# Kernel optimization log

Hardware: AMD Instinct MI355X
Metric: run time of the kernel (lower is better)

## Reference

```python
import jax, jax.numpy as jnp
import numpy as np

WINDOW_SIZE = 35

def setup_inputs() -> dict:
    key = jax.random.key(0)
    k1, k2 = jax.random.split(key)
    B, T, U = 4096, WINDOW_SIZE, 1024
    x = jax.random.normal(k1, (B, T, U), dtype=jnp.float32)
    # nn.Linear(units*2, units): weight [units, units*2], bias [units]
    W = jax.random.normal(k2, (U, 2 * U), dtype=jnp.float32) * (1.0 / np.sqrt(2 * U))
    b = jnp.zeros((U,), dtype=jnp.float32)
    return {"x": x, "W": W, "b": b}

def reference(x, W, b):
    # x: [B, T, U]; hidden init zeros [B, U]
    B, T, U = x.shape
    # split weight into input part and hidden part (concat order: [x_t, h])
    Wx = W[:, :U]   # [U, U]
    Wh = W[:, U:]   # [U, U]

    def step(h, x_t):
        # out = relu([x_t, h] @ W^T + b)
        h_new = jax.nn.relu(x_t @ Wx.T + h @ Wh.T + b)
        return h_new, None

    h0 = jnp.zeros((B, U), dtype=x.dtype)
    x_time_major = jnp.swapaxes(x, 0, 1)  # [T, B, U]
    h_final, _ = jax.lax.scan(step, h0, x_time_major)
    return h_final
```

## Files before the change

kernel.cpp:

```cpp
#include <hip/hip_runtime.h>


typedef __bf16 bf16;
typedef __bf16 bf16x8 __attribute__((ext_vector_type(8)));
typedef __bf16 bf16x4 __attribute__((ext_vector_type(4)));
typedef float f32x4 __attribute__((ext_vector_type(4)));

#define B_N 4096
#define T_N 35
#define U_N 1024
#define XROW (T_N * U_N)
#define BU (B_N * U_N)

#define AS1CP(p) ((const __attribute__((address_space(1))) void*)(p))
#define AS3CP(p) ((__attribute__((address_space(3))) void*)(p))

__global__ __launch_bounds__(256) void pack_w(const float* __restrict__ W,
                                              bf16* __restrict__ Wxb,
                                              bf16* __restrict__ Whb) {
  int i = (blockIdx.x * 256 + threadIdx.x) * 4;
  int n = i >> 10, k = i & 1023;
  f32x4 a = *(const f32x4*)(W + (size_t)n * 2048 + k);
  f32x4 b = *(const f32x4*)(W + (size_t)n * 2048 + 1024 + k);
  bf16x4 av = { (bf16)a.x, (bf16)a.y, (bf16)a.z, (bf16)a.w };
  bf16x4 bv = { (bf16)b.x, (bf16)b.y, (bf16)b.z, (bf16)b.w };
  *(bf16x4*)(Wxb + i) = av;
  *(bf16x4*)(Whb + i) = bv;
}

__global__ __launch_bounds__(256) void z_gemm(
    const float* __restrict__ x, const bf16* __restrict__ Wxb,
    const float* __restrict__ bias, bf16* __restrict__ Zb)
{
  __shared__ bf16 As[128 * 64];
  __shared__ bf16 Bs[128 * 64];

  const int tid = threadIdx.x;
  const int w = tid >> 6, l = tid & 63;
  const int mt = blockIdx.y;
  const int t = mt >> 5;
  const int row0 = (mt & 31) << 7;
  const int col0 = blockIdx.x << 7;
  const int wm = w & 1, wn = w >> 1;
  const int lq = l >> 4, lm = l & 15;
  const int lrow8 = l >> 3, lc = l & 7;
  const int clog = lc ^ lrow8;

  f32x4 acc[4][4] = {};
  const float* xbase = x + (size_t)row0 * XROW + (size_t)t * U_N;

  for (int kk = 0; kk < 1024; kk += 64) {
#pragma unroll
    for (int r = 0; r < 4; ++r) {
      int nr = w * 32 + r * 8;
      const bf16* g = Wxb + (size_t)(col0 + nr + lrow8) * U_N + kk + clog * 8;
      __builtin_amdgcn_global_load_lds(AS1CP(g), AS3CP(Bs + nr * 64), 16, 0, 0);
    }
#pragma unroll
    for (int i = 0; i < 4; ++i) {
      int row = i * 32 + (tid >> 3);
      int c = tid & 7;
      const float* g = xbase + (size_t)row * XROW + kk + c * 8;
      f32x4 f0 = *(const f32x4*)g;
      f32x4 f1 = *(const f32x4*)(g + 4);
      bf16x8 v = { (bf16)f0.x, (bf16)f0.y, (bf16)f0.z, (bf16)f0.w,
                   (bf16)f1.x, (bf16)f1.y, (bf16)f1.z, (bf16)f1.w };
      *(bf16x8*)(As + row * 64 + ((c ^ (row & 7)) << 3)) = v;
    }
    __syncthreads();

#pragma unroll
    for (int kq = 0; kq < 2; ++kq) {
      bf16x8 af[4], bfr[4];
#pragma unroll
      for (int mi = 0; mi < 4; ++mi) {
        int r = wm * 64 + mi * 16 + lm;
        af[mi] = *(const bf16x8*)(As + r * 64 + (((kq * 4 + lq) ^ (r & 7)) << 3));
      }
#pragma unroll
      for (int ni = 0; ni < 4; ++ni) {
        int r = wn * 64 + ni * 16 + lm;
        bfr[ni] = *(const bf16x8*)(Bs + r * 64 + (((kq * 4 + lq) ^ (r & 7)) << 3));
      }
#pragma unroll
      for (int mi = 0; mi < 4; ++mi)
#pragma unroll
        for (int ni = 0; ni < 4; ++ni)
          acc[mi][ni] = __builtin_amdgcn_mfma_f32_16x16x32_bf16(af[mi], bfr[ni],
                                                                acc[mi][ni], 0, 0, 0);
    }
    __syncthreads();
  }

#pragma unroll
  for (int ni = 0; ni < 4; ++ni) {
    int col = col0 + wn * 64 + ni * 16 + lm;
    float bv = bias[col];
#pragma unroll
    for (int mi = 0; mi < 4; ++mi) {
      int rbase = row0 + wm * 64 + mi * 16 + lq * 4;
#pragma unroll
      for (int i = 0; i < 4; ++i)
        Zb[(size_t)t * BU + (size_t)(rbase + i) * U_N + col] = (bf16)(acc[mi][ni][i] + bv);
    }
  }
}

__global__ __launch_bounds__(256) void rnn_step(
    const bf16* __restrict__ hin, const bf16* __restrict__ Whb,
    const bf16* __restrict__ Zt, bf16* __restrict__ hout,
    float* __restrict__ out)
{
  __shared__ bf16 As[128 * 64];
  __shared__ bf16 Bs[64 * 64];

  const int tid = threadIdx.x;
  const int w = tid >> 6, l = tid & 63;
  const int col0 = blockIdx.x << 6;
  const int row0 = blockIdx.y << 7;
  const int wm = w & 1, wn = w >> 1;
  const int lq = l >> 4, lm = l & 15;
  const int lrow8 = l >> 3, lc = l & 7;
  const int clog = lc ^ lrow8;

  f32x4 acc[4][2] = {};

  for (int kk = 0; kk < 1024; kk += 64) {
#pragma unroll
    for (int r = 0; r < 4; ++r) {
      int nr = w * 32 + r * 8;
      const bf16* g = hin + (size_t)(row0 + nr + lrow8) * U_N + kk + clog * 8;
      __builtin_amdgcn_global_load_lds(AS1CP(g), AS3CP(As + nr * 64), 16, 0, 0);
    }
#pragma unroll
    for (int r = 0; r < 2; ++r) {
      int nr = w * 16 + r * 8;
      const bf16* g = Whb + (size_t)(col0 + nr + lrow8) * U_N + kk + clog * 8;
      __builtin_amdgcn_global_load_lds(AS1CP(g), AS3CP(Bs + nr * 64), 16, 0, 0);
    }
    __syncthreads();

#pragma unroll
    for (int kq = 0; kq < 2; ++kq) {
      bf16x8 af[4], bfr[2];
#pragma unroll
      for (int mi = 0; mi < 4; ++mi) {
        int r = wm * 64 + mi * 16 + lm;
        af[mi] = *(const bf16x8*)(As + r * 64 + (((kq * 4 + lq) ^ (r & 7)) << 3));
      }
#pragma unroll
      for (int ni = 0; ni < 2; ++ni) {
        int r = wn * 32 + ni * 16 + lm;
        bfr[ni] = *(const bf16x8*)(Bs + r * 64 + (((kq * 4 + lq) ^ (r & 7)) << 3));
      }
#pragma unroll
      for (int mi = 0; mi < 4; ++mi)
#pragma unroll
        for (int ni = 0; ni < 2; ++ni)
          acc[mi][ni] = __builtin_amdgcn_mfma_f32_16x16x32_bf16(af[mi], bfr[ni],
                                                                acc[mi][ni], 0, 0, 0);
    }
    __syncthreads();
  }

#pragma unroll
  for (int ni = 0; ni < 2; ++ni) {
    int col = col0 + wn * 32 + ni * 16 + lm;
#pragma unroll
    for (int mi = 0; mi < 4; ++mi) {
      int rbase = row0 + wm * 64 + mi * 16 + lq * 4;
#pragma unroll
      for (int i = 0; i < 4; ++i) {
        int row = rbase + i;
        float v = acc[mi][ni][i] + (float)Zt[(size_t)row * U_N + col];
        v = v > 0.f ? v : 0.f;
        hout[(size_t)row * U_N + col] = (bf16)v;
        if (out) out[(size_t)row * U_N + col] = v;
      }
    }
  }
}

extern "C" void kernel_launch(void* const* d_in, const int* in_sizes, int n_in,
                              void* d_out, int out_size, void* d_ws, size_t ws_size,
                              hipStream_t stream) {
  const float* x    = (const float*)d_in[0];
  const float* W    = (const float*)d_in[1];
  const float* bias = (const float*)d_in[2];
  float* out = (float*)d_out;

  char* ws = (char*)d_ws;
  bf16* Wxb = (bf16*)ws;
  bf16* Whb = (bf16*)(ws + ((size_t)2 << 20));
  bf16* h0  = (bf16*)(ws + ((size_t)4 << 20));
  bf16* h1  = (bf16*)(ws + ((size_t)12 << 20));
  bf16* Zb  = (bf16*)(ws + ((size_t)32 << 20));

  pack_w<<<1024, 256, 0, stream>>>(W, Wxb, Whb);
  hipMemsetAsync(h0, 0, (size_t)BU * sizeof(bf16), stream);

  z_gemm<<<dim3(8, 1120), 256, 0, stream>>>(x, Wxb, bias, Zb);

  bf16* bufs[2] = { h0, h1 };
  for (int t = 0; t < T_N; ++t) {
    bf16* hin  = bufs[t & 1];
    bf16* hout = bufs[(t + 1) & 1];
    float* o   = (t == T_N - 1) ? out : nullptr;
    rnn_step<<<dim3(16, 32), 256, 0, stream>>>(hin, Whb, Zb + (size_t)t * BU, hout, o);
  }
}
```

Baseline: 2.237 ms.

## Fuse input projection and recurrence into one persistent cooperative kernel

Replaces the separate Z precompute GEMM and per-timestep launches with one cooperative persistent kernel. Each step computes [x_t, h] @ W^T over K=2048 with double-buffered LDS and split-K across two wave groups, and a global atomic barrier separates timesteps. This removes the Z intermediate's write and read traffic plus per-step launch overhead. In exchange the x projection is now on the serial per-step path, and the spin barrier adds synchronization cost.

```diff
diff --git a/kernel.cpp b/kernel.cpp
--- a/kernel.cpp
+++ b/kernel.cpp
@@ -9,174 +9,189 @@
 #define B_N 4096
 #define T_N 35
 #define U_N 1024
+#define K2 2048
 #define XROW (T_N * U_N)
-#define BU (B_N * U_N)
 
 #define AS1CP(p) ((const __attribute__((address_space(1))) void*)(p))
 #define AS3CP(p) ((__attribute__((address_space(3))) void*)(p))
 
 __global__ __launch_bounds__(256) void pack_w(const float* __restrict__ W,
-                                              bf16* __restrict__ Wxb,
-                                              bf16* __restrict__ Whb) {
+                                              bf16* __restrict__ Wb) {
   int i = (blockIdx.x * 256 + threadIdx.x) * 4;
-  int n = i >> 10, k = i & 1023;
-  f32x4 a = *(const f32x4*)(W + (size_t)n * 2048 + k);
-  f32x4 b = *(const f32x4*)(W + (size_t)n * 2048 + 1024 + k);
-  bf16x4 av = { (bf16)a.x, (bf16)a.y, (bf16)a.z, (bf16)a.w };
-  bf16x4 bv = { (bf16)b.x, (bf16)b.y, (bf16)b.z, (bf16)b.w };
-  *(bf16x4*)(Wxb + i) = av;
-  *(bf16x4*)(Whb + i) = bv;
+  f32x4 a = *(const f32x4*)(W + i);
+  bf16x4 v = { (bf16)a.x, (bf16)a.y, (bf16)a.z, (bf16)a.w };
+  *(bf16x4*)(Wb + i) = v;
 }
 
-__global__ __launch_bounds__(256) void z_gemm(
-    const float* __restrict__ x, const bf16* __restrict__ Wxb,
-    const float* __restrict__ bias, bf16* __restrict__ Zb)
+__global__ __launch_bounds__(512, 1) void rnn_fused(
+    const float* __restrict__ x, const bf16* __restrict__ Wb,
+    const float* __restrict__ bias, bf16* __restrict__ hA,
+    bf16* __restrict__ hB, float* __restrict__ out,
+    unsigned* __restrict__ bar, int t0, int t1)
 {
-  __shared__ bf16 As[128 * 64];
-  __shared__ bf16 Bs[128 * 64];
+  __shared__ __align__(16) bf16 smem[2][2][128 * 64];
 
   const int tid = threadIdx.x;
   const int w = tid >> 6, l = tid & 63;
-  const int mt = blockIdx.y;
-  const int t = mt >> 5;
-  const int row0 = (mt & 31) << 7;
-  const int col0 = blockIdx.x << 7;
-  const int wm = w & 1, wn = w >> 1;
+  const int L = blockIdx.x;
+  const int rg = (L & 7) * 4 + ((L >> 3) >> 3);
+  const int cg = (L >> 3) & 7;
+  const int r0 = rg << 7;
+  const int c0 = cg << 7;
+
+  const int s = w & 3;
+  const int g = w >> 2;
+  const int wm = s & 1, wn = s >> 1;
   const int lq = l >> 4, lm = l & 15;
-  const int lrow8 = l >> 3, lc = l & 7;
-  const int clog = lc ^ lrow8;
-
-  f32x4 acc[4][4] = {};
-  const float* xbase = x + (size_t)row0 * XROW + (size_t)t * U_N;
-
-  for (int kk = 0; kk < 1024; kk += 64) {
-#pragma unroll
-    for (int r = 0; r < 4; ++r) {
-      int nr = w * 32 + r * 8;
-      const bf16* g = Wxb + (size_t)(col0 + nr + lrow8) * U_N + kk + clog * 8;
-      __builtin_amdgcn_global_load_lds(AS1CP(g), AS3CP(Bs + nr * 64), 16, 0, 0);
-    }
-#pragma unroll
-    for (int i = 0; i < 4; ++i) {
-      int row = i * 32 + (tid >> 3);
-      int c = tid & 7;
-      const float* g = xbase + (size_t)row * XROW + kk + c * 8;
-      f32x4 f0 = *(const f32x4*)g;
-      f32x4 f1 = *(const f32x4*)(g + 4);
-      bf16x8 v = { (bf16)f0.x, (bf16)f0.y, (bf16)f0.z, (bf16)f0.w,
-                   (bf16)f1.x, (bf16)f1.y, (bf16)f1.z, (bf16)f1.w };
-      *(bf16x8*)(As + row * 64 + ((c ^ (row & 7)) << 3)) = v;
-    }
-    __syncthreads();
-
-#pragma unroll
-    for (int kq = 0; kq < 2; ++kq) {
-      bf16x8 af[4], bfr[4];
-#pragma unroll
-      for (int mi = 0; mi < 4; ++mi) {
-        int r = wm * 64 + mi * 16 + lm;
-        af[mi] = *(const bf16x8*)(As + r * 64 + (((kq * 4 + lq) ^ (r & 7)) << 3));
-      }
-#pragma unroll
-      for (int ni = 0; ni < 4; ++ni) {
-        int r = wn * 64 + ni * 16 + lm;
-        bfr[ni] = *(const bf16x8*)(Bs + r * 64 + (((kq * 4 + lq) ^ (r & 7)) << 3));
-      }
-#pragma unroll
-      for (int mi = 0; mi < 4; ++mi)
-#pragma unroll
-        for (int ni = 0; ni < 4; ++ni)
-          acc[mi][ni] = __builtin_amdgcn_mfma_f32_16x16x32_bf16(af[mi], bfr[ni],
-                                                                acc[mi][ni], 0, 0, 0);
-    }
-    __syncthreads();
-  }
-
-#pragma unroll
-  for (int ni = 0; ni < 4; ++ni) {
-    int col = col0 + wn * 64 + ni * 16 + lm;
-    float bv = bias[col];
-#pragma unroll
-    for (int mi = 0; mi < 4; ++mi) {
-      int rbase = row0 + wm * 64 + mi * 16 + lq * 4;
-#pragma unroll
-      for (int i = 0; i < 4; ++i)
-        Zb[(size_t)t * BU + (size_t)(rbase + i) * U_N + col] = (bf16)(acc[mi][ni][i] + bv);
-    }
-  }
-}
-
-__global__ __launch_bounds__(256) void rnn_step(
-    const bf16* __restrict__ hin, const bf16* __restrict__ Whb,
-    const bf16* __restrict__ Zt, bf16* __restrict__ hout,
-    float* __restrict__ out)
-{
-  __shared__ bf16 As[128 * 64];
-  __shared__ bf16 Bs[64 * 64];
-
-  const int tid = threadIdx.x;
-  const int w = tid >> 6, l = tid & 63;
-  const int col0 = blockIdx.x << 6;
-  const int row0 = blockIdx.y << 7;
-  const int wm = w & 1, wn = w >> 1;
-  const int lq = l >> 4, lm = l & 15;
-  const int lrow8 = l >> 3, lc = l & 7;
-  const int clog = lc ^ lrow8;
-
-  f32x4 acc[4][2] = {};
-
-  for (int kk = 0; kk < 1024; kk += 64) {
-#pragma unroll
-    for (int r = 0; r < 4; ++r) {
-      int nr = w * 32 + r * 8;
-      const bf16* g = hin + (size_t)(row0 + nr + lrow8) * U_N + kk + clog * 8;
-      __builtin_amdgcn_global_load_lds(AS1CP(g), AS3CP(As + nr * 64), 16, 0, 0);
-    }
+  const int lrow8 = l >> 3;
+  const int clog = (l & 7) ^ lrow8;
+
+  const int xrow = tid >> 2;
+  const int xc2 = tid & 3;
+  const float* xrowp = x + (size_t)(r0 + xrow) * XROW + xc2 * 16;
+
+  float bv[4];
+#pragma unroll
+  for (int ni = 0; ni < 4; ++ni) bv[ni] = bias[c0 + wn * 64 + ni * 16 + lm];
+
+  for (int t = t0; t < t1; ++t) {
+    const bf16* hin = (t & 1) ? hB : hA;
+    bf16* hout = (t & 1) ? hA : hB;
+    const int kend = (t == 0) ? 1024 : K2;
+    const float* xb = xrowp + (size_t)t * U_N;
+
+    f32x4 acc[4][4] = {};
+
 #pragma unroll
     for (int r = 0; r < 2; ++r) {
       int nr = w * 16 + r * 8;
-      const bf16* g = Whb + (size_t)(col0 + nr + lrow8) * U_N + kk + clog * 8;
-      __builtin_amdgcn_global_load_lds(AS1CP(g), AS3CP(Bs + nr * 64), 16, 0, 0);
+      const bf16* gb = Wb + (size_t)(c0 + nr + lrow8) * K2 + clog * 8;
+      __builtin_amdgcn_global_load_lds(AS1CP(gb), AS3CP(&smem[0][1][nr * 64]), 16, 0, 0);
+    }
+    {
+      f32x4 f0 = *(const f32x4*)(xb);
+      f32x4 f1 = *(const f32x4*)(xb + 4);
+      f32x4 f2 = *(const f32x4*)(xb + 8);
+      f32x4 f3 = *(const f32x4*)(xb + 12);
+      bf16x8 v0 = { (bf16)f0.x, (bf16)f0.y, (bf16)f0.z, (bf16)f0.w,
+                    (bf16)f1.x, (bf16)f1.y, (bf16)f1.z, (bf16)f1.w };
+      bf16x8 v1 = { (bf16)f2.x, (bf16)f2.y, (bf16)f2.z, (bf16)f2.w,
+                    (bf16)f3.x, (bf16)f3.y, (bf16)f3.z, (bf16)f3.w };
+      *(bf16x8*)(&smem[0][0][xrow * 64 + (((xc2 << 1) ^ (xrow & 7)) << 3)]) = v0;
+      *(bf16x8*)(&smem[0][0][xrow * 64 + ((((xc2 << 1) | 1) ^ (xrow & 7)) << 3)]) = v1;
     }
     __syncthreads();
 
-#pragma unroll
-    for (int kq = 0; kq < 2; ++kq) {
-      bf16x8 af[4], bfr[2];
-#pragma unroll
-      for (int mi = 0; mi < 4; ++mi) {
-        int r = wm * 64 + mi * 16 + lm;
-        af[mi] = *(const bf16x8*)(As + r * 64 + (((kq * 4 + lq) ^ (r & 7)) << 3));
-      }
-#pragma unroll
-      for (int ni = 0; ni < 2; ++ni) {
-        int r = wn * 32 + ni * 16 + lm;
-        bfr[ni] = *(const bf16x8*)(Bs + r * 64 + (((kq * 4 + lq) ^ (r & 7)) << 3));
-      }
+    int cur = 0;
+    for (int kk = 0; kk < kend; kk += 64) {
+      const int nkk = kk + 64;
+      const bool hasnext = nkk < kend;
+      const bool nx = hasnext && (nkk < 1024);
+      const bool nh = hasnext && (nkk >= 1024);
+      const int nxt = cur ^ 1;
+
+      f32x4 f0, f1, f2, f3;
+      if (nx) {
+        const float* gx = xb + nkk;
+        f0 = *(const f32x4*)(gx);
+        f1 = *(const f32x4*)(gx + 4);
+        f2 = *(const f32x4*)(gx + 8);
+        f3 = *(const f32x4*)(gx + 12);
+      }
+      if (hasnext) {
+#pragma unroll
+        for (int r = 0; r < 2; ++r) {
+          int nr = w * 16 + r * 8;
+          const bf16* gb = Wb + (size_t)(c0 + nr + lrow8) * K2 + nkk + clog * 8;
+          __builtin_amdgcn_global_load_lds(AS1CP(gb), AS3CP(&smem[nxt][1][nr * 64]), 16, 0, 0);
+        }
+      }
+      if (nh) {
+#pragma unroll
+        for (int r = 0; r < 2; ++r) {
+          int nr = w * 16 + r * 8;
+          const bf16* gh = hin + (size_t)(r0 + nr + lrow8) * U_N + (nkk - 1024) + clog * 8;
+          __builtin_amdgcn_global_load_lds(AS1CP(gh), AS3CP(&smem[nxt][0][nr * 64]), 16, 0, 0);
+        }
+      }
+
+      {
+        const bf16* As = &smem[cur][0][0];
+        const bf16* Bs = &smem[cur][1][0];
+        bf16x8 af[4], bfr[4];
+#pragma unroll
+        for (int mi = 0; mi < 4; ++mi) {
+          int r = wm * 64 + mi * 16 + lm;
+          af[mi] = *(const bf16x8*)(As + r * 64 + ((((g << 2) + lq) ^ (r & 7)) << 3));
+        }
+#pragma unroll
+        for (int ni = 0; ni < 4; ++ni) {
+          int c = wn * 64 + ni * 16 + lm;
+          bfr[ni] = *(const bf16x8*)(Bs + c * 64 + ((((g << 2) + lq) ^ (c & 7)) << 3));
+        }
+#pragma unroll
+        for (int mi = 0; mi < 4; ++mi)
+#pragma unroll
+          for (int ni = 0; ni < 4; ++ni)
+            acc[mi][ni] = __builtin_amdgcn_mfma_f32_16x16x32_bf16(af[mi], bfr[ni],
+                                                                  acc[mi][ni], 0, 0, 0);
+      }
+
+      if (nx) {
+        bf16x8 v0 = { (bf16)f0.x, (bf16)f0.y, (bf16)f0.z, (bf16)f0.w,
+                      (bf16)f1.x, (bf16)f1.y, (bf16)f1.z, (bf16)f1.w };
+        bf16x8 v1 = { (bf16)f2.x, (bf16)f2.y, (bf16)f2.z, (bf16)f2.w,
+                      (bf16)f3.x, (bf16)f3.y, (bf16)f3.z, (bf16)f3.w };
+        *(bf16x8*)(&smem[nxt][0][xrow * 64 + (((xc2 << 1) ^ (xrow & 7)) << 3)]) = v0;
+        *(bf16x8*)(&smem[nxt][0][xrow * 64 + ((((xc2 << 1) | 1) ^ (xrow & 7)) << 3)]) = v1;
+      }
+      __syncthreads();
+      cur = nxt;
+    }
+
+    float* red = (float*)&smem[0][0][0];
+    if (g == 1) {
 #pragma unroll
       for (int mi = 0; mi < 4; ++mi)
 #pragma unroll
-        for (int ni = 0; ni < 2; ++ni)
-          acc[mi][ni] = __builtin_amdgcn_mfma_f32_16x16x32_bf16(af[mi], bfr[ni],
-                                                                acc[mi][ni], 0, 0, 0);
+        for (int ni = 0; ni < 4; ++ni)
+          *(f32x4*)(red + (size_t)(s * 16 + mi * 4 + ni) * 256 + l * 4) = acc[mi][ni];
     }
     __syncthreads();
-  }
-
-#pragma unroll
-  for (int ni = 0; ni < 2; ++ni) {
-    int col = col0 + wn * 32 + ni * 16 + lm;
-#pragma unroll
-    for (int mi = 0; mi < 4; ++mi) {
-      int rbase = row0 + wm * 64 + mi * 16 + lq * 4;
-#pragma unroll
-      for (int i = 0; i < 4; ++i) {
-        int row = rbase + i;
-        float v = acc[mi][ni][i] + (float)Zt[(size_t)row * U_N + col];
-        v = v > 0.f ? v : 0.f;
-        hout[(size_t)row * U_N + col] = (bf16)v;
-        if (out) out[(size_t)row * U_N + col] = v;
-      }
+    if (g == 0) {
+#pragma unroll
+      for (int mi = 0; mi < 4; ++mi)
+#pragma unroll
+        for (int ni = 0; ni < 4; ++ni)
+          acc[mi][ni] += *(const f32x4*)(red + (size_t)(s * 16 + mi * 4 + ni) * 256 + l * 4);
+
+#pragma unroll
+      for (int ni = 0; ni < 4; ++ni) {
+        int col = c0 + wn * 64 + ni * 16 + lm;
+#pragma unroll
+        for (int mi = 0; mi < 4; ++mi) {
+          int rbase = r0 + wm * 64 + mi * 16 + lq * 4;
+#pragma unroll
+          for (int i = 0; i < 4; ++i) {
+            float v = acc[mi][ni][i] + bv[ni];
+            v = v > 0.f ? v : 0.f;
+            hout[(size_t)(rbase + i) * U_N + col] = (bf16)v;
+            if (t == T_N - 1) out[(size_t)(rbase + i) * U_N + col] = v;
+          }
+        }
+      }
+    }
+
+    if (t + 1 < t1) {
+      __syncthreads();
+      if (tid == 0) {
+        __threadfence();
+        atomicAdd(bar, 1u);
+        unsigned tgt = (unsigned)(t + 1 - t0) * 256u;
+        while (atomicAdd(bar, 0u) < tgt) __builtin_amdgcn_s_sleep(2);
+      }
+      __syncthreads();
+      __threadfence();
     }
   }
 }
@@ -190,22 +205,23 @@
   float* out = (float*)d_out;
 
   char* ws = (char*)d_ws;
-  bf16* Wxb = (bf16*)ws;
-  bf16* Whb = (bf16*)(ws + ((size_t)2 << 20));
-  bf16* h0  = (bf16*)(ws + ((size_t)4 << 20));
-  bf16* h1  = (bf16*)(ws + ((size_t)12 << 20));
-  bf16* Zb  = (bf16*)(ws + ((size_t)32 << 20));
-
-  pack_w<<<1024, 256, 0, stream>>>(W, Wxb, Whb);
-  hipMemsetAsync(h0, 0, (size_t)BU * sizeof(bf16), stream);
-
-  z_gemm<<<dim3(8, 1120), 256, 0, stream>>>(x, Wxb, bias, Zb);
-
-  bf16* bufs[2] = { h0, h1 };
-  for (int t = 0; t < T_N; ++t) {
-    bf16* hin  = bufs[t & 1];
-    bf16* hout = bufs[(t + 1) & 1];
-    float* o   = (t == T_N - 1) ? out : nullptr;
-    rnn_step<<<dim3(16, 32), 256, 0, stream>>>(hin, Whb, Zb + (size_t)t * BU, hout, o);
+  bf16* Wb = (bf16*)ws;
+  bf16* hA = (bf16*)(ws + ((size_t)4 << 20));
+  bf16* hB = (bf16*)(ws + ((size_t)12 << 20));
+  unsigned* bar = (unsigned*)(ws + ((size_t)20 << 20));
+
+  pack_w<<<2048, 256, 0, stream>>>(W, Wb);
+  hipMemsetAsync(bar, 0, sizeof(unsigned), stream);
+
+  int t0 = 0, t1 = T_N;
+  void* args[] = { (void*)&x, (void*)&Wb, (void*)&bias, (void*)&hA, (void*)&hB,
+                   (void*)&out, (void*)&bar, (void*)&t0, (void*)&t1 };
+  hipError_t err = hipLaunchCooperativeKernel((const void*)rnn_fused, dim3(256),
+                                              dim3(512), args, 0, stream);
+  if (err != hipSuccess) {
+    (void)hipGetLastError();
+    for (int t = 0; t < T_N; ++t)
+      rnn_fused<<<dim3(256), dim3(512), 0, stream>>>(x, Wb, bias, hA, hB, out,
+                                                     bar, t, t + 1);
   }
 }
```

New measurement: 3.411 ms. +52.5%, slower.
